# Kernel tuning notes

Measured on AMD Instinct MI355X. Metric: run time of the kernel, lower is better.

## Reference

```python
import jax, jax.numpy as jnp
import numpy as np

B, C_IN, H, W = 32, 512, 56, 56   # post-backbone feature map (resnet18, chan=64 -> 512 feats)
C_ENC = 64                         # topk_enc_chan
K = 256                            # topk_pxls_nb


def setup_inputs() -> dict:
    key = jax.random.key(0)
    k1, k2, k3 = jax.random.split(key, 3)
    return {
        "features": jax.random.normal(k1, (B, C_IN, H, W), jnp.float32),
        "conv_w": jax.random.normal(k2, (C_ENC, C_IN), jnp.float32) * 0.02,
        "conv_b": jax.random.normal(k3, (C_ENC,), jnp.float32) * 0.02,
    }


def reference(features, conv_w, conv_b):
    # 1x1 conv: [B,C_IN,H,W] -> [B,C_ENC,H,W]
    feats = jnp.einsum('bchw,oc->bohw', features, conv_w) + conv_b[None, :, None, None]
    b, c, h, w = feats.shape
    flat = feats.reshape(b, c, h * w)                      # [B,C,HW]
    # per-pixel squared L2 norm over channels
    norm = jnp.sum(flat * flat, axis=1)                    # [B,HW]
    _, idx = jax.lax.top_k(norm, K)                        # [B,K]
    abs_ = idx % w                                          # x coord
    ord_ = idx // w                                         # y coord
    # gather selected pixel features: mapToList equivalent -> [B,K,C]
    feat_list = jnp.take_along_axis(flat, idx[:, None, :], axis=2).transpose(0, 2, 1)
    x_out = feat_list.mean(axis=1)                         # [B,C]
    # scatter 1s into sparse attention map
    sw = jnp.zeros((b, h * w), feats.dtype).at[jnp.arange(b)[:, None], idx].set(1.0)
    sw = sw.reshape(b, 1, h, w)
    depth = jnp.zeros((b, K, 1), feats.dtype)
    points = jnp.concatenate(
        [abs_[..., None].astype(feats.dtype), ord_[..., None].astype(feats.dtype), depth, feat_list],
        axis=-1)                                           # [B,K,3+C]
    return (x_out, sw, points)
```

## Files before the change

kernel.cpp:

```cpp
#include <hip/hip_runtime.h>

#define B_     32
#define C_IN_  512
#define H_     56
#define W_     56
#define HW_    (H_ * W_)
#define C_ENC_ 64
#define K_     256
#define BHW_   (B_ * HW_)
#define PTS_ROW_ (3 + C_ENC_)

__global__ __launch_bounds__(256) void k_transpose_w(
        const float* __restrict__ w, float* __restrict__ wt) {
    int i = blockIdx.x * 256 + threadIdx.x;
    if (i < C_ENC_ * C_IN_) {
        int o = i / C_IN_;
        int c = i % C_IN_;
        wt[c * C_ENC_ + o] = w[i];
    }
}

__global__ __launch_bounds__(256, 8) void k_conv_norm(
        const float* __restrict__ F, const float* __restrict__ wt,
        const float* __restrict__ bias, float* __restrict__ norms,
        float* __restrict__ feats) {
    __shared__ float accs[64][65];

    int t = threadIdx.x;
    int pix_l = t & 63;
    int g = __builtin_amdgcn_readfirstlane(t >> 6);
    int pb = blockIdx.x;
    int b = pb / 49;
    int pix0 = (pb % 49) * 64;

    const float* f  = F + (size_t)b * (C_IN_ * HW_) + pix0 + pix_l;
    const float* wg = wt + g * 16;

    float acc[16];
    #pragma unroll
    for (int o = 0; o < 16; ++o) acc[o] = bias[g * 16 + o];

    float x[8];
    #pragma unroll
    for (int u = 0; u < 8; ++u) x[u] = f[(size_t)u * HW_];

    for (int c0 = 0; c0 < C_IN_; c0 += 8) {
        float xn[4];
        int cA = (c0 + 8) & 511;
        #pragma unroll
        for (int u = 0; u < 4; ++u) xn[u] = f[(size_t)(cA + u) * HW_];
        #pragma unroll
        for (int u = 0; u < 4; ++u)
            #pragma unroll
            for (int o = 0; o < 16; ++o)
                acc[o] = fmaf(x[u], wg[(c0 + u) * C_ENC_ + o], acc[o]);
        #pragma unroll
        for (int u = 0; u < 4; ++u) x[u] = xn[u];
        int cB = (c0 + 12) & 511;
        #pragma unroll
        for (int u = 0; u < 4; ++u) xn[u] = f[(size_t)(cB + u) * HW_];
        #pragma unroll
        for (int u = 0; u < 4; ++u)
            #pragma unroll
            for (int o = 0; o < 16; ++o)
                acc[o] = fmaf(x[4 + u], wg[(c0 + 4 + u) * C_ENC_ + o], acc[o]);
        #pragma unroll
        for (int u = 0; u < 4; ++u) x[4 + u] = xn[u];
    }

    #pragma unroll
    for (int o = 0; o < 16; ++o)
        feats[(size_t)(b * C_ENC_ + g * 16 + o) * HW_ + pix0 + pix_l] = acc[o];

    #pragma unroll
    for (int o = 0; o < 16; ++o) accs[pix_l][g * 16 + o] = acc[o];
    __syncthreads();

    if (t < 64) {
        float nrm = 0.0f;
        #pragma unroll
        for (int o = 0; o < C_ENC_; ++o)
            nrm = fmaf(accs[t][o], accs[t][o], nrm);
        norms[b * HW_ + pix0 + t] = nrm;
    }
}

__global__ __launch_bounds__(512) void k_topk(
        const float* __restrict__ norms, unsigned int* __restrict__ topk,
        float* __restrict__ sw_out) {
    __shared__ unsigned int keys[HW_];
    __shared__ unsigned int hist[256];
    __shared__ unsigned long long sortbuf[512];
    __shared__ unsigned int s_prefix, s_need, s_cnt;
    __shared__ unsigned char flags[HW_];

    int b = blockIdx.x;
    int t = threadIdx.x;
    const float* nb = norms + b * HW_;

    for (int i = t; i < HW_; i += 512) {
        keys[i] = __float_as_uint(nb[i]);
        flags[i] = 0;
    }
    if (t == 0) { s_prefix = 0u; s_need = K_; s_cnt = 0u; }
    for (int i = t; i < 512; i += 512) sortbuf[i] = ~0ULL;

    for (int r = 0; r < 4; ++r) {
        if (t < 256) hist[t] = 0u;
        __syncthreads();
        unsigned int pfx = s_prefix;
        int shift = 24 - 8 * r;
        for (int i = t; i < HW_; i += 512) {
            unsigned int k = keys[i];
            bool ok = (r == 0) || ((k >> (32 - 8 * r)) == pfx);
            if (ok) atomicAdd(&hist[(k >> shift) & 0xFFu], 1u);
        }
        __syncthreads();
        if (t < 64) {
            unsigned int h0 = hist[4 * t + 0];
            unsigned int h1 = hist[4 * t + 1];
            unsigned int h2 = hist[4 * t + 2];
            unsigned int h3 = hist[4 * t + 3];
            unsigned int tot = h0 + h1 + h2 + h3;
            unsigned int suf = tot;
            #pragma unroll
            for (int off = 1; off < 64; off <<= 1) {
                unsigned int v = __shfl_down(suf, off);
                suf += (t + off < 64) ? v : 0u;
            }
            unsigned int g0 = suf;
            unsigned int g1 = suf - h0;
            unsigned int g2 = g1 - h1;
            unsigned int g3 = g2 - h2;
            unsigned int g4 = g3 - h3;
            unsigned int need = s_need;
            if (g0 >= need && g1 < need) { s_prefix = (pfx << 8) | (4u*t+0u); s_need = need - g1; }
            if (g1 >= need && g2 < need) { s_prefix = (pfx << 8) | (4u*t+1u); s_need = need - g2; }
            if (g2 >= need && g3 < need) { s_prefix = (pfx << 8) | (4u*t+2u); s_need = need - g3; }
            if (g3 >= need && g4 < need) { s_prefix = (pfx << 8) | (4u*t+3u); s_need = need - g4; }
        }
        __syncthreads();
    }
    unsigned int T = s_prefix;

    for (int i = t; i < HW_; i += 512) {
        unsigned int k = keys[i];
        if (k >= T) {
            unsigned int pos = atomicAdd(&s_cnt, 1u);
            if (pos < 512)
                sortbuf[pos] = ((unsigned long long)(~k) << 32) | (unsigned int)i;
        }
    }
    __syncthreads();

    for (int kk = 2; kk <= 512; kk <<= 1) {
        for (int j = kk >> 1; j > 0; j >>= 1) {
            int ixj = t ^ j;
            if (ixj > t) {
                unsigned long long a = sortbuf[t], c = sortbuf[ixj];
                bool up = ((t & kk) == 0);
                if ((a > c) == up) { sortbuf[t] = c; sortbuf[ixj] = a; }
            }
            __syncthreads();
        }
    }

    if (t < K_) {
        unsigned long long e = sortbuf[t];
        unsigned int idx = (unsigned int)(e & 0xFFFFFFFFu);
        topk[b * K_ + t] = idx;
        flags[idx] = 1;
    }
    __syncthreads();

    float* swb = sw_out + b * HW_;
    for (int i = t; i < HW_; i += 512)
        swb[i] = flags[i] ? 1.0f : 0.0f;
}

__global__ __launch_bounds__(64) void k_points(
        const float* __restrict__ feats, const unsigned int* __restrict__ topk,
        float* __restrict__ points) {
    int bk = blockIdx.x;
    int b = bk >> 8;
    int o = threadIdx.x;
    unsigned int p = topk[bk];

    float v = feats[(size_t)(b * C_ENC_ + o) * HW_ + p];
    float* row = points + (size_t)bk * PTS_ROW_;
    row[3 + o] = v;
    if (o == 0) {
        row[0] = (float)(p % W_);
        row[1] = (float)(p / W_);
        row[2] = 0.0f;
    }
}

__global__ __launch_bounds__(64) void k_xout(
        const float* __restrict__ feats, const unsigned int* __restrict__ topk,
        float* __restrict__ xout) {
    __shared__ unsigned int sidx[K_];
    int b = blockIdx.x;
    int t = threadIdx.x;
    for (int r = t; r < K_; r += 64) sidx[r] = topk[b * K_ + r];
    __syncthreads();

    const float* fb = feats + (size_t)(b * C_ENC_ + t) * HW_;
    float s = 0.0f;
    #pragma unroll 8
    for (int k = 0; k < K_; ++k) s += fb[sidx[k]];
    xout[b * C_ENC_ + t] = s * (1.0f / K_);
}

extern "C" void kernel_launch(void* const* d_in, const int* in_sizes, int n_in,
                              void* d_out, int out_size, void* d_ws, size_t ws_size,
                              hipStream_t stream) {
    const float* F    = (const float*)d_in[0];
    const float* w    = (const float*)d_in[1];
    const float* bias = (const float*)d_in[2];

    float* out    = (float*)d_out;
    float* xout   = out;
    float* sw     = out + B_ * C_ENC_;
    float* points = sw + BHW_;

    float* feats         = (float*)d_ws;
    float* wt            = feats + (size_t)B_ * C_ENC_ * HW_;
    float* norms         = wt + C_IN_ * C_ENC_;
    unsigned int* topk   = (unsigned int*)(norms + BHW_);

    k_transpose_w<<<128, 256, 0, stream>>>(w, wt);
    k_conv_norm  <<<BHW_ / 64, 256, 0, stream>>>(F, wt, bias, norms, feats);
    k_topk       <<<B_, 512, 0, stream>>>(norms, topk, sw);
    k_points     <<<B_ * K_, 64, 0, stream>>>(feats, topk, points);
    k_xout       <<<B_, 64, 0, stream>>>(feats, topk, xout);
}
```

Before: 178.8 us.

## Share conv input loads across waves via async global-to-LDS triple buffering

The 1x1 conv kernel now stages each 16-channel chunk of input pixels into a triple-buffered LDS ring using global_load_lds. Each wave loads a quarter of the chunk, where before every wave read all channels itself, which removes the 4x redundant global reads per block. The norm is computed from per-wave partial sums instead of re-reading all 64 accumulators from LDS. This adds a block barrier every chunk and drops the occupancy hint in launch bounds.

```diff
diff --git a/kernel.cpp b/kernel.cpp
--- a/kernel.cpp
+++ b/kernel.cpp
@@ -10,6 +10,10 @@
 #define BHW_   (B_ * HW_)
 #define PTS_ROW_ (3 + C_ENC_)
 
+#define CHUNK_ 16
+#define NSTEP_ (C_IN_ / CHUNK_)
+#define NBUF_  3
+
 __global__ __launch_bounds__(256) void k_transpose_w(
         const float* __restrict__ w, float* __restrict__ wt) {
     int i = blockIdx.x * 256 + threadIdx.x;
@@ -20,11 +24,18 @@
     }
 }
 
-__global__ __launch_bounds__(256, 8) void k_conv_norm(
+__device__ __forceinline__ void gload_lds4(const float* g, float* l) {
+    __builtin_amdgcn_global_load_lds(
+        (const __attribute__((address_space(1))) void*)g,
+        (__attribute__((address_space(3))) void*)l, 4, 0, 0);
+}
+
+__global__ __launch_bounds__(256) void k_conv_norm(
         const float* __restrict__ F, const float* __restrict__ wt,
         const float* __restrict__ bias, float* __restrict__ norms,
         float* __restrict__ feats) {
-    __shared__ float accs[64][65];
+    __shared__ float xbuf[NBUF_][CHUNK_][64];
+    __shared__ float nrmp[64][4];
 
     int t = threadIdx.x;
     int pix_l = t & 63;
@@ -40,47 +51,47 @@
     #pragma unroll
     for (int o = 0; o < 16; ++o) acc[o] = bias[g * 16 + o];
 
-    float x[8];
-    #pragma unroll
-    for (int u = 0; u < 8; ++u) x[u] = f[(size_t)u * HW_];
-
-    for (int c0 = 0; c0 < C_IN_; c0 += 8) {
-        float xn[4];
-        int cA = (c0 + 8) & 511;
+    #pragma unroll
+    for (int u = 0; u < 4; ++u)
+        gload_lds4(f + (size_t)(g * 4 + u) * HW_, &xbuf[0][g * 4 + u][0]);
+
+    for (int s = 0; s < NSTEP_; ++s) {
+        if (s + 1 < NSTEP_) {
+            int cn = (s + 1) * CHUNK_ + g * 4;
+            int slot = (s + 1) % NBUF_;
+            #pragma unroll
+            for (int u = 0; u < 4; ++u)
+                gload_lds4(f + (size_t)(cn + u) * HW_, &xbuf[slot][g * 4 + u][0]);
+            asm volatile("s_waitcnt vmcnt(4)" ::: "memory");
+        } else {
+            asm volatile("s_waitcnt vmcnt(0)" ::: "memory");
+        }
+        __builtin_amdgcn_sched_barrier(0);
+        __syncthreads();
+
+        int slot = s % NBUF_;
+        int cb = s * CHUNK_;
         #pragma unroll
-        for (int u = 0; u < 4; ++u) xn[u] = f[(size_t)(cA + u) * HW_];
-        #pragma unroll
-        for (int u = 0; u < 4; ++u)
+        for (int cl = 0; cl < CHUNK_; ++cl) {
+            float x = xbuf[slot][cl][pix_l];
             #pragma unroll
             for (int o = 0; o < 16; ++o)
-                acc[o] = fmaf(x[u], wg[(c0 + u) * C_ENC_ + o], acc[o]);
-        #pragma unroll
-        for (int u = 0; u < 4; ++u) x[u] = xn[u];
-        int cB = (c0 + 12) & 511;
-        #pragma unroll
-        for (int u = 0; u < 4; ++u) xn[u] = f[(size_t)(cB + u) * HW_];
-        #pragma unroll
-        for (int u = 0; u < 4; ++u)
-            #pragma unroll
-            for (int o = 0; o < 16; ++o)
-                acc[o] = fmaf(x[4 + u], wg[(c0 + 4 + u) * C_ENC_ + o], acc[o]);
-        #pragma unroll
-        for (int u = 0; u < 4; ++u) x[4 + u] = xn[u];
+                acc[o] = fmaf(x, wg[(cb + cl) * C_ENC_ + o], acc[o]);
+        }
     }
 
     #pragma unroll
     for (int o = 0; o < 16; ++o)
         feats[(size_t)(b * C_ENC_ + g * 16 + o) * HW_ + pix0 + pix_l] = acc[o];
 
-    #pragma unroll
-    for (int o = 0; o < 16; ++o) accs[pix_l][g * 16 + o] = acc[o];
+    float p = 0.0f;
+    #pragma unroll
+    for (int o = 0; o < 16; ++o) p = fmaf(acc[o], acc[o], p);
+    nrmp[pix_l][g] = p;
     __syncthreads();
 
     if (t < 64) {
-        float nrm = 0.0f;
-        #pragma unroll
-        for (int o = 0; o < C_ENC_; ++o)
-            nrm = fmaf(accs[t][o], accs[t][o], nrm);
+        float nrm = ((nrmp[t][0] + nrmp[t][1]) + nrmp[t][2]) + nrmp[t][3];
         norms[b * HW_ + pix0 + t] = nrm;
     }
 }
```

Measured after the change: 163.1 us. 8.8% less time.
